# Kernel optimization log

Hardware: AMD Instinct MI355X
Metric: run time of the kernel (lower is better)

The kernel has to match this reference:

```python
import jax, jax.numpy as jnp
import numpy as np

N = 20000      # nodes
E = 160000     # edges (before self-loops)
B = 128        # graphs in batch
NEG_SLOPE = 0.2


def gat_layer(x, src, dst, W, a_src, a_dst, b):
    # x: [N, Cin]; W: [Cin, H*C]; a_src/a_dst: [H, C]; b: [C]
    H, C = a_src.shape
    n = x.shape[0]
    xw = (x @ W).reshape(n, H, C)                      # [N, H, C]
    alpha_src = jnp.sum(xw * a_src, axis=-1)           # [N, H]
    alpha_dst = jnp.sum(xw * a_dst, axis=-1)           # [N, H]
    e = jax.nn.leaky_relu(alpha_src[src] + alpha_dst[dst], NEG_SLOPE)  # [Etot, H]
    # numerically stable segment softmax over edges grouped by target node
    m = jax.ops.segment_max(e, dst, num_segments=n)    # [N, H]
    m = jnp.where(jnp.isfinite(m), m, 0.0)
    ex = jnp.exp(e - m[dst])                           # [Etot, H]
    den = jax.ops.segment_sum(ex, dst, num_segments=n) # [N, H]
    alpha = ex / (den[dst] + 1e-16)                    # [Etot, H]
    out = jax.ops.segment_sum(alpha[:, :, None] * xw[src], dst, num_segments=n)  # [N, H, C]
    return out.mean(axis=1) + b                        # concat=False -> head mean + bias


def setup_inputs() -> dict:
    key = jax.random.key(0)
    ks = jax.random.split(key, 12)
    s = 0.05
    x = jax.random.normal(ks[0], (N, 768), dtype=jnp.float32)
    edge_index = jax.random.randint(ks[1], (2, E), 0, N, dtype=jnp.int64)
    batch = jnp.sort(jax.random.randint(ks[2], (N,), 0, B, dtype=jnp.int64))
    W1 = jax.random.normal(ks[3], (768, 4 * 512), dtype=jnp.float32) * s
    a_src1 = jax.random.normal(ks[4], (4, 512), dtype=jnp.float32) * s
    a_dst1 = jax.random.normal(ks[5], (4, 512), dtype=jnp.float32) * s
    b1 = jnp.zeros((512,), dtype=jnp.float32)
    W2 = jax.random.normal(ks[6], (512, 4 * 256), dtype=jnp.float32) * s
    a_src2 = jax.random.normal(ks[7], (4, 256), dtype=jnp.float32) * s
    a_dst2 = jax.random.normal(ks[8], (4, 256), dtype=jnp.float32) * s
    b2 = jnp.zeros((256,), dtype=jnp.float32)
    fcW = jax.random.normal(ks[9], (256, 2), dtype=jnp.float32) * s
    fcb = jnp.zeros((2,), dtype=jnp.float32)
    return {"x": x, "edge_index": edge_index, "batch": batch,
            "W1": W1, "a_src1": a_src1, "a_dst1": a_dst1, "b1": b1,
            "W2": W2, "a_src2": a_src2, "a_dst2": a_dst2, "b2": b2,
            "fcW": fcW, "fcb": fcb}


def reference(x, edge_index, batch, W1, a_src1, a_dst1, b1, W2, a_src2, a_dst2, b2, fcW, fcb):
    n = x.shape[0]
    loops = jnp.arange(n, dtype=edge_index.dtype)      # GATConv adds self-loops by default
    src = jnp.concatenate([edge_index[0], loops])
    dst = jnp.concatenate([edge_index[1], loops])
    h = gat_layer(x, src, dst, W1, a_src1, a_dst1, b1)   # [N, 512]
    h = gat_layer(h, src, dst, W2, a_src2, a_dst2, b2)   # [N, 256]
    sums = jax.ops.segment_sum(h, batch, num_segments=B)                     # [B, 256]
    cnt = jax.ops.segment_sum(jnp.ones((n,), h.dtype), batch, num_segments=B)
    g = sums / jnp.maximum(cnt, 1.0)[:, None]            # scatter_mean
    return g @ fcW + fcb                                  # [B, 2]
```

## Files before the change

### kernel.cpp

```cpp
#include <hip/hip_runtime.h>

#define NN    20000
#define NE    160000
#define NETOT 180000
#define NB    128

typedef __attribute__((ext_vector_type(4))) float f32x4;
typedef __attribute__((ext_vector_type(8))) short s16x8;

__device__ __forceinline__ unsigned short f2bf(float f){
  unsigned u = __float_as_uint(f);
  return (unsigned short)((u + 0x7FFFu + ((u >> 16) & 1u)) >> 16);
}
__device__ __forceinline__ float bf2f(unsigned short h){
  return __uint_as_float(((unsigned)h) << 16);
}
__device__ __forceinline__ void gload16(const void* g, void* l){
  __builtin_amdgcn_global_load_lds((const __attribute__((address_space(1))) void*)g,
                                   (__attribute__((address_space(3))) void*)l, 16, 0, 0);
}

__global__ void k_cvt(const float* __restrict__ in, unsigned short* __restrict__ outp, int n4){
  int i = blockIdx.x * blockDim.x + threadIdx.x;
  if (i >= n4) return;
  float4 v = ((const float4*)in)[i];
  ushort4 h;
  h.x = f2bf(v.x); h.y = f2bf(v.y); h.z = f2bf(v.z); h.w = f2bf(v.w);
  ((ushort4*)outp)[i] = h;
}

__global__ void k_tcvt(const float* __restrict__ W, unsigned short* __restrict__ T, int K, int N){
  __shared__ float tile[32][33];
  int tx = threadIdx.x, ty = threadIdx.y;
  int n = blockIdx.x * 32 + tx, k = blockIdx.y * 32 + ty;
  tile[ty][tx] = W[(size_t)k * N + n];
  __syncthreads();
  int n2 = blockIdx.x * 32 + ty, k2 = blockIdx.y * 32 + tx;
  T[(size_t)n2 * K + k2] = f2bf(tile[tx][ty]);
}

__global__ __launch_bounds__(256, 2)
void gemm_bf16(const unsigned short* __restrict__ A, const unsigned short* __restrict__ BT,
               unsigned short* __restrict__ C, int M, int N, int K, int ntile){
  __shared__ unsigned short lds[24576];
  const int t = threadIdx.x;
  const int lane = t & 63;
  const int w = t >> 6;
  const int wr = w >> 1, wc = w & 1;
  const int mt = blockIdx.x / ntile, nt = blockIdx.x % ntile;
  const int m0 = mt << 7, n0 = nt << 8;
  const int NK = K >> 5;

  int offA[4], offB[8];
#pragma unroll
  for (int mi = 0; mi < 4; ++mi){
    int row = wr * 64 + mi * 16 + (lane & 15);
    offA[mi] = row * 32 + (((lane >> 4) ^ ((row >> 1) & 3)) << 3);
  }
#pragma unroll
  for (int ni = 0; ni < 8; ++ni){
    int row = wc * 128 + ni * 16 + (lane & 15);
    offB[ni] = 4096 + row * 32 + (((lane >> 4) ^ ((row >> 1) & 3)) << 3);
  }

  const unsigned short* srcA[2]; int dstA[2];
#pragma unroll
  for (int j = 0; j < 2; ++j){
    int rA = w * 32 + j * 16 + (lane >> 2);
    int gr = m0 + rA; if (gr >= M) gr = M - 1;
    srcA[j] = A + (size_t)gr * K + (((lane & 3) ^ ((rA >> 1) & 3)) << 3);
    dstA[j] = w * 1024 + j * 512 + lane * 8;
  }
  const unsigned short* srcB[4]; int dstB[4];
#pragma unroll
  for (int j = 0; j < 4; ++j){
    int rB = w * 64 + j * 16 + (lane >> 2);
    srcB[j] = BT + (size_t)(n0 + rB) * K + (((lane & 3) ^ ((rB >> 1) & 3)) << 3);
    dstB[j] = 4096 + w * 2048 + j * 512 + lane * 8;
  }

#define STAGE(ks, bo) { int _k = (ks) << 5; \
    gload16(srcA[0] + _k, &lds[(bo) + dstA[0]]); \
    gload16(srcA[1] + _k, &lds[(bo) + dstA[1]]); \
    gload16(srcB[0] + _k, &lds[(bo) + dstB[0]]); \
    gload16(srcB[1] + _k, &lds[(bo) + dstB[1]]); \
    gload16(srcB[2] + _k, &lds[(bo) + dstB[2]]); \
    gload16(srcB[3] + _k, &lds[(bo) + dstB[3]]); }

  f32x4 acc[4][8];
#pragma unroll
  for (int i = 0; i < 4; ++i)
#pragma unroll
    for (int j = 0; j < 8; ++j) acc[i][j] = (f32x4){0.f, 0.f, 0.f, 0.f};

  STAGE(0, 0);
  asm volatile("s_waitcnt vmcnt(0)" ::: "memory");
  __builtin_amdgcn_sched_barrier(0);
  __builtin_amdgcn_s_barrier();
  __builtin_amdgcn_sched_barrier(0);

  for (int ks = 0; ks < NK; ++ks){
    const int bo = (ks & 1) * 12288;
    s16x8 av[4], bv[8];
#pragma unroll
    for (int i = 0; i < 4; ++i) av[i] = *(const s16x8*)&lds[bo + offA[i]];
#pragma unroll
    for (int i = 0; i < 8; ++i) bv[i] = *(const s16x8*)&lds[bo + offB[i]];
    if (ks + 1 < NK) STAGE(ks + 1, 12288 - bo);
    __builtin_amdgcn_s_setprio(1);
#pragma unroll
    for (int mi = 0; mi < 4; ++mi)
#pragma unroll
      for (int ni = 0; ni < 8; ++ni)
        acc[mi][ni] = __builtin_amdgcn_mfma_f32_16x16x32_bf16(av[mi], bv[ni], acc[mi][ni], 0, 0, 0);
    __builtin_amdgcn_s_setprio(0);
    asm volatile("s_waitcnt vmcnt(0)" ::: "memory");
    __builtin_amdgcn_sched_barrier(0);
    __builtin_amdgcn_s_barrier();
    __builtin_amdgcn_sched_barrier(0);
  }
#undef STAGE

#pragma unroll
  for (int h = 0; h < 2; ++h){
    if (wr == h){
#pragma unroll
      for (int mi = 0; mi < 4; ++mi)
#pragma unroll
        for (int ni = 0; ni < 8; ++ni)
#pragma unroll
          for (int r = 0; r < 4; ++r){
            int rl = mi * 16 + ((lane >> 4) << 2) + r;
            int col = wc * 128 + ni * 16 + (lane & 15);
            int byte = (rl * 512 + col * 2) ^ (((rl >> 2) & 3) << 5);
            *(unsigned short*)((char*)lds + byte) = f2bf(acc[mi][ni][r]);
          }
    }
    __syncthreads();
#pragma unroll
    for (int it = 0; it < 8; ++it){
      int idx = it * 256 + t;
      int rl = idx >> 5, c16 = idx & 31;
      int byte = (rl * 512 + c16 * 16) ^ (((rl >> 2) & 3) << 5);
      s16x8 v = *(const s16x8*)((const char*)lds + byte);
      int grow = m0 + h * 64 + rl;
      if (grow < M)
        *(s16x8*)(C + (size_t)grow * N + n0 + c16 * 8) = v;
    }
    __syncthreads();
  }
}

template<int C>
__global__ void k_alpha(const unsigned short* __restrict__ xw, const float* __restrict__ a_src,
                        const float* __restrict__ a_dst, float* __restrict__ asrc,
                        float* __restrict__ adst){
  const int n = blockIdx.x, t = threadIdx.x;
  constexpr int W = C / 8;
  const int head = (t * 8) / C;
  const int c0 = (t * 8) % C;
  s16x8 v = *(const s16x8*)(xw + (size_t)n * 4 * C + t * 8);
  float4 s0 = *(const float4*)(a_src + head * C + c0);
  float4 s1 = *(const float4*)(a_src + head * C + c0 + 4);
  float4 d0 = *(const float4*)(a_dst + head * C + c0);
  float4 d1 = *(const float4*)(a_dst + head * C + c0 + 4);
  float f[8];
#pragma unroll
  for (int j = 0; j < 8; ++j) f[j] = bf2f((unsigned short)v[j]);
  float ps = f[0]*s0.x + f[1]*s0.y + f[2]*s0.z + f[3]*s0.w
           + f[4]*s1.x + f[5]*s1.y + f[6]*s1.z + f[7]*s1.w;
  float pd = f[0]*d0.x + f[1]*d0.y + f[2]*d0.z + f[3]*d0.w
           + f[4]*d1.x + f[5]*d1.y + f[6]*d1.z + f[7]*d1.w;
#pragma unroll
  for (int off = W / 2; off; off >>= 1){
    ps += __shfl_xor(ps, off);
    pd += __shfl_xor(pd, off);
  }
  if ((t & (W - 1)) == 0){
    asrc[n * 4 + head] = ps;
    adst[n * 4 + head] = pd;
  }
}

__global__ void k_count(const int* __restrict__ ei, int* __restrict__ counts){
  int e = blockIdx.x * blockDim.x + threadIdx.x;
  if (e >= NETOT) return;
  int d = (e < NE) ? ei[NE + e] : (e - NE);
  atomicAdd(&counts[d], 1);
}
__global__ void k_scan(const int* __restrict__ counts, int* __restrict__ row_ptr,
                       int* __restrict__ cursor){
  __shared__ int lds[1024];
  int t = threadIdx.x;
  int base = 0;
  for (int c0 = 0; c0 < NN; c0 += 1024){
    int i = c0 + t;
    int v = (i < NN) ? counts[i] : 0;
    __syncthreads();
    lds[t] = v;
    __syncthreads();
    for (int off = 1; off < 1024; off <<= 1){
      int x = (t >= off) ? lds[t - off] : 0;
      __syncthreads();
      lds[t] += x;
      __syncthreads();
    }
    int excl = base + lds[t] - v;
    if (i < NN){ row_ptr[i] = excl; cursor[i] = excl; }
    base += lds[1023];
  }
  if (t == 0) row_ptr[NN] = base;
}
__global__ void k_scatter(const int* __restrict__ ei, int* __restrict__ cursor,
                          int* __restrict__ csr_src){
  int e = blockIdx.x * blockDim.x + threadIdx.x;
  if (e >= NETOT) return;
  int s, d;
  if (e < NE){ s = ei[e]; d = ei[NE + e]; } else { s = d = e - NE; }
  int pos = atomicAdd(&cursor[d], 1);
  csr_src[pos] = s;
}

__global__ void k_edge(const int* __restrict__ rp, const int* __restrict__ csrc,
                       const float* __restrict__ asrc, const float* __restrict__ adst,
                       float* __restrict__ ex, float* __restrict__ den){
  int n = blockIdx.x * 4 + (threadIdx.x >> 6);
  if (n >= NN) return;
  int lane = threadIdx.x & 63;
  int beg = rp[n], end = rp[n + 1];
  float4 ad = ((const float4*)adst)[n];
  float mx0 = -1e30f, mx1 = -1e30f, mx2 = -1e30f, mx3 = -1e30f;
  for (int i = beg + lane; i < end; i += 64){
    int s = csrc[i];
    float4 as = ((const float4*)asrc)[s];
    float v0 = as.x + ad.x; v0 = v0 > 0.f ? v0 : 0.2f * v0; mx0 = fmaxf(mx0, v0);
    float v1 = as.y + ad.y; v1 = v1 > 0.f ? v1 : 0.2f * v1; mx1 = fmaxf(mx1, v1);
    float v2 = as.z + ad.z; v2 = v2 > 0.f ? v2 : 0.2f * v2; mx2 = fmaxf(mx2, v2);
    float v3 = as.w + ad.w; v3 = v3 > 0.f ? v3 : 0.2f * v3; mx3 = fmaxf(mx3, v3);
  }
#pragma unroll
  for (int off = 32; off; off >>= 1){
    mx0 = fmaxf(mx0, __shfl_xor(mx0, off));
    mx1 = fmaxf(mx1, __shfl_xor(mx1, off));
    mx2 = fmaxf(mx2, __shfl_xor(mx2, off));
    mx3 = fmaxf(mx3, __shfl_xor(mx3, off));
  }
  float s0 = 0.f, s1 = 0.f, s2 = 0.f, s3 = 0.f;
  for (int i = beg + lane; i < end; i += 64){
    int s = csrc[i];
    float4 as = ((const float4*)asrc)[s];
    float v0 = as.x + ad.x; v0 = v0 > 0.f ? v0 : 0.2f * v0;
    float v1 = as.y + ad.y; v1 = v1 > 0.f ? v1 : 0.2f * v1;
    float v2 = as.z + ad.z; v2 = v2 > 0.f ? v2 : 0.2f * v2;
    float v3 = as.w + ad.w; v3 = v3 > 0.f ? v3 : 0.2f * v3;
    float e0 = __expf(v0 - mx0), e1 = __expf(v1 - mx1);
    float e2 = __expf(v2 - mx2), e3 = __expf(v3 - mx3);
    s0 += e0; s1 += e1; s2 += e2; s3 += e3;
    ((float4*)ex)[i] = make_float4(e0, e1, e2, e3);
  }
#pragma unroll
  for (int off = 32; off; off >>= 1){
    s0 += __shfl_xor(s0, off);
    s1 += __shfl_xor(s1, off);
    s2 += __shfl_xor(s2, off);
    s3 += __shfl_xor(s3, off);
  }
  if (lane == 0) ((float4*)den)[n] = make_float4(s0, s1, s2, s3);
}

template<int C, bool BF16OUT>
__global__ void k_agg(const unsigned short* __restrict__ xw, const int* __restrict__ row_ptr,
                      const int* __restrict__ csr_src,
                      const float* __restrict__ ex, const float* __restrict__ den,
                      const float* __restrict__ bias, void* __restrict__ outp){
  const int n = blockIdx.x, t = threadIdx.x;
  constexpr int LPH = C / 8;
  const int h = t / LPH, c0 = (t % LPH) * 8;
  __shared__ float red[4][C];
  float rdh = 1.f / (den[n * 4 + h] + 1e-16f);
  float acc[8] = {};
  int beg = row_ptr[n], end = row_ptr[n + 1];
  const unsigned short* xwh = xw + h * C + c0;
  for (int i = beg; i < end; ++i){
    int s = csr_src[i];
    float aa = ex[i * 4 + h] * rdh;
    s16x8 v = *(const s16x8*)(xwh + (size_t)s * 4 * C);
#pragma unroll
    for (int j = 0; j < 8; ++j) acc[j] += aa * bf2f((unsigned short)v[j]);
  }
#pragma unroll
  for (int j = 0; j < 8; ++j) red[h][c0 + j] = acc[j];
  __syncthreads();
  if (t < LPH){
    int cc = t * 8;
    float o[8];
#pragma unroll
    for (int j = 0; j < 8; ++j)
      o[j] = 0.25f * (red[0][cc + j] + red[1][cc + j] + red[2][cc + j] + red[3][cc + j])
           + bias[cc + j];
    if (BF16OUT){
      union { unsigned short u[8]; s16x8 v; } pk;
#pragma unroll
      for (int j = 0; j < 8; ++j) pk.u[j] = f2bf(o[j]);
      *(s16x8*)((unsigned short*)outp + (size_t)n * C + cc) = pk.v;
    } else {
      float* op = (float*)outp + (size_t)n * C + cc;
      ((float4*)op)[0] = make_float4(o[0], o[1], o[2], o[3]);
      ((float4*)op)[1] = make_float4(o[4], o[5], o[6], o[7]);
    }
  }
}

__global__ void k_pool(const float* __restrict__ h2, const int* __restrict__ batch,
                       float* __restrict__ sums, int* __restrict__ cnt){
  int n0 = blockIdx.x * 64;
  int t = threadIdx.x;
  int nend = n0 + 64; if (nend > NN) nend = NN;
  int cur = batch[n0];
  float acc = 0.f; int run = 0;
  for (int n = n0; n < nend; ++n){
    int b = batch[n];
    if (b != cur){
      atomicAdd(&sums[cur * 256 + t], acc);
      if (t == 0) atomicAdd(&cnt[cur], run);
      acc = 0.f; run = 0; cur = b;
    }
    acc += h2[(size_t)n * 256 + t];
    run++;
  }
  atomicAdd(&sums[cur * 256 + t], acc);
  if (t == 0) atomicAdd(&cnt[cur], run);
}

__global__ void k_fc(const float* __restrict__ sums, const int* __restrict__ cnt,
                     const float* __restrict__ fcW, const float* __restrict__ fcb,
                     float* __restrict__ out){
  int b = blockIdx.x, t = threadIdx.x;
  int c = cnt[b]; if (c < 1) c = 1;
  float inv = 1.f / (float)c;
  float v = sums[b * 256 + t] * inv;
  float p0 = v * fcW[t * 2];
  float p1 = v * fcW[t * 2 + 1];
#pragma unroll
  for (int off = 32; off; off >>= 1){
    p0 += __shfl_xor(p0, off);
    p1 += __shfl_xor(p1, off);
  }
  __shared__ float r0[4], r1[4];
  if ((t & 63) == 0){ r0[t >> 6] = p0; r1[t >> 6] = p1; }
  __syncthreads();
  if (t == 0){
    out[b * 2 + 0] = r0[0] + r0[1] + r0[2] + r0[3] + fcb[0];
    out[b * 2 + 1] = r1[0] + r1[1] + r1[2] + r1[3] + fcb[1];
  }
}

extern "C" void kernel_launch(void* const* d_in, const int* in_sizes, int n_in,
                              void* d_out, int out_size, void* d_ws, size_t ws_size,
                              hipStream_t stream){
  const float* x      = (const float*)d_in[0];
  const int*   ei     = (const int*)d_in[1];
  const int*   batch  = (const int*)d_in[2];
  const float* W1     = (const float*)d_in[3];
  const float* a_src1 = (const float*)d_in[4];
  const float* a_dst1 = (const float*)d_in[5];
  const float* b1     = (const float*)d_in[6];
  const float* W2     = (const float*)d_in[7];
  const float* a_src2 = (const float*)d_in[8];
  const float* a_dst2 = (const float*)d_in[9];
  const float* b2     = (const float*)d_in[10];
  const float* fcW    = (const float*)d_in[11];
  const float* fcb    = (const float*)d_in[12];
  float* out = (float*)d_out;
  (void)in_sizes; (void)n_in; (void)out_size; (void)ws_size;

  char* ws = (char*)d_ws;
  size_t off = 0;
  auto take = [&](size_t bytes) -> char* {
    char* p = ws + off;
    off += (bytes + 255) & ~(size_t)255;
    return p;
  };
  char* slab0 = take(81920000);
  unsigned short* xw1 = (unsigned short*)slab0;
  unsigned short* xw2 = (unsigned short*)slab0;
  unsigned short* x_bf  = (unsigned short*)take(30720000);
  unsigned short* h1_bf = (unsigned short*)take(20480000);
  float*          h2    = (float*)take(20480000);
  unsigned short* W1T = (unsigned short*)take(3145728);
  unsigned short* W2T = (unsigned short*)take(1048576);
  float* asrc   = (float*)take(320000);
  float* adst   = (float*)take(320000);
  float* den    = (float*)take(320000);
  float* ex     = (float*)take((size_t)NETOT * 16);
  int* counts   = (int*)take(80004);
  int* row_ptr  = (int*)take(80004);
  int* cursor   = (int*)take(80004);
  int* csr_src  = (int*)take(720000);
  float* sums   = (float*)take(131072);
  int* cnt      = (int*)take(512);

  const int egrid = (NETOT + 255) / 256;

  hipMemsetAsync(counts, 0, NN * 4, stream);
  k_count<<<egrid, 256, 0, stream>>>(ei, counts);
  k_scan<<<1, 1024, 0, stream>>>(counts, row_ptr, cursor);
  k_scatter<<<egrid, 256, 0, stream>>>(ei, cursor, csr_src);

  k_cvt<<<(3840000 + 255) / 256, 256, 0, stream>>>(x, x_bf, 3840000);
  k_tcvt<<<dim3(2048 / 32, 768 / 32), dim3(32, 32), 0, stream>>>(W1, W1T, 768, 2048);
  gemm_bf16<<<157 * 8, 256, 0, stream>>>(x_bf, W1T, xw1, NN, 2048, 768, 8);
  k_alpha<512><<<NN, 256, 0, stream>>>(xw1, a_src1, a_dst1, asrc, adst);
  k_edge<<<(NN + 3) / 4, 256, 0, stream>>>(row_ptr, csr_src, asrc, adst, ex, den);
  k_agg<512, true><<<NN, 256, 0, stream>>>(xw1, row_ptr, csr_src, ex, den, b1, h1_bf);

  k_tcvt<<<dim3(1024 / 32, 512 / 32), dim3(32, 32), 0, stream>>>(W2, W2T, 512, 1024);
  gemm_bf16<<<157 * 4, 256, 0, stream>>>(h1_bf, W2T, xw2, NN, 1024, 512, 4);
  k_alpha<256><<<NN, 128, 0, stream>>>(xw2, a_src2, a_dst2, asrc, adst);
  k_edge<<<(NN + 3) / 4, 256, 0, stream>>>(row_ptr, csr_src, asrc, adst, ex, den);
  k_agg<256, false><<<NN, 128, 0, stream>>>(xw2, row_ptr, csr_src, ex, den, b2, h2);

  hipMemsetAsync(sums, 0, 131072, stream);
  hipMemsetAsync(cnt, 0, 512, stream);
  k_pool<<<(NN + 63) / 64, 256, 0, stream>>>(h2, batch, sums, cnt);
  k_fc<<<NB, 256, 0, stream>>>(sums, cnt, fcW, fcb, out);
}
```

Before: 540.2 us.

## Aggregate raw inputs per head before projecting, folding head-mean into GEMM

Reorders each GAT layer algebraically. Attention logits come from x·(W·a), so a small projected vector replaces the full x@W. Aggregation runs on the raw input features per head (width 4·Cin). A single GEMM with a head-concatenated weight scaled by 0.25 and a fused bias then performs the head mean. This drops the ex/den buffers and the separate edge and alpha passes, and fuses the softmax into aggregation. In exchange the aggregated intermediate is larger (N×4·Cin in bf16), the GEMM K grows, and the GEMM grid for layer 2 has only 157 blocks. The layer-2 output is also stored in bf16, which costs precision.

```diff
diff --git a/kernel.cpp b/kernel.cpp
--- a/kernel.cpp
+++ b/kernel.cpp
@@ -29,156 +29,66 @@
   ((ushort4*)outp)[i] = h;
 }
 
-__global__ void k_tcvt(const float* __restrict__ W, unsigned short* __restrict__ T, int K, int N){
-  __shared__ float tile[32][33];
-  int tx = threadIdx.x, ty = threadIdx.y;
-  int n = blockIdx.x * 32 + tx, k = blockIdx.y * 32 + ty;
-  tile[ty][tx] = W[(size_t)k * N + n];
+__global__ void k_va(const float* __restrict__ W, const float* __restrict__ aS,
+                     const float* __restrict__ aD, float* __restrict__ va, int K, int C){
+  __shared__ float a_s[2048], a_d[2048];
+  int t = threadIdx.x;
+  int HC = 4 * C;
+  for (int i = t; i < HC; i += 256){ a_s[i] = aS[i]; a_d[i] = aD[i]; }
   __syncthreads();
-  int n2 = blockIdx.x * 32 + ty, k2 = blockIdx.y * 32 + tx;
-  T[(size_t)n2 * K + k2] = f2bf(tile[tx][ty]);
-}
-
-__global__ __launch_bounds__(256, 2)
-void gemm_bf16(const unsigned short* __restrict__ A, const unsigned short* __restrict__ BT,
-               unsigned short* __restrict__ C, int M, int N, int K, int ntile){
-  __shared__ unsigned short lds[24576];
-  const int t = threadIdx.x;
-  const int lane = t & 63;
-  const int w = t >> 6;
-  const int wr = w >> 1, wc = w & 1;
-  const int mt = blockIdx.x / ntile, nt = blockIdx.x % ntile;
-  const int m0 = mt << 7, n0 = nt << 8;
-  const int NK = K >> 5;
-
-  int offA[4], offB[8];
-#pragma unroll
-  for (int mi = 0; mi < 4; ++mi){
-    int row = wr * 64 + mi * 16 + (lane & 15);
-    offA[mi] = row * 32 + (((lane >> 4) ^ ((row >> 1) & 3)) << 3);
-  }
-#pragma unroll
-  for (int ni = 0; ni < 8; ++ni){
-    int row = wc * 128 + ni * 16 + (lane & 15);
-    offB[ni] = 4096 + row * 32 + (((lane >> 4) ^ ((row >> 1) & 3)) << 3);
-  }
-
-  const unsigned short* srcA[2]; int dstA[2];
-#pragma unroll
-  for (int j = 0; j < 2; ++j){
-    int rA = w * 32 + j * 16 + (lane >> 2);
-    int gr = m0 + rA; if (gr >= M) gr = M - 1;
-    srcA[j] = A + (size_t)gr * K + (((lane & 3) ^ ((rA >> 1) & 3)) << 3);
-    dstA[j] = w * 1024 + j * 512 + lane * 8;
-  }
-  const unsigned short* srcB[4]; int dstB[4];
-#pragma unroll
-  for (int j = 0; j < 4; ++j){
-    int rB = w * 64 + j * 16 + (lane >> 2);
-    srcB[j] = BT + (size_t)(n0 + rB) * K + (((lane & 3) ^ ((rB >> 1) & 3)) << 3);
-    dstB[j] = 4096 + w * 2048 + j * 512 + lane * 8;
-  }
-
-#define STAGE(ks, bo) { int _k = (ks) << 5; \
-    gload16(srcA[0] + _k, &lds[(bo) + dstA[0]]); \
-    gload16(srcA[1] + _k, &lds[(bo) + dstA[1]]); \
-    gload16(srcB[0] + _k, &lds[(bo) + dstB[0]]); \
-    gload16(srcB[1] + _k, &lds[(bo) + dstB[1]]); \
-    gload16(srcB[2] + _k, &lds[(bo) + dstB[2]]); \
-    gload16(srcB[3] + _k, &lds[(bo) + dstB[3]]); }
-
-  f32x4 acc[4][8];
-#pragma unroll
-  for (int i = 0; i < 4; ++i)
-#pragma unroll
-    for (int j = 0; j < 8; ++j) acc[i][j] = (f32x4){0.f, 0.f, 0.f, 0.f};
-
-  STAGE(0, 0);
-  asm volatile("s_waitcnt vmcnt(0)" ::: "memory");
-  __builtin_amdgcn_sched_barrier(0);
-  __builtin_amdgcn_s_barrier();
-  __builtin_amdgcn_sched_barrier(0);
-
-  for (int ks = 0; ks < NK; ++ks){
-    const int bo = (ks & 1) * 12288;
-    s16x8 av[4], bv[8];
-#pragma unroll
-    for (int i = 0; i < 4; ++i) av[i] = *(const s16x8*)&lds[bo + offA[i]];
-#pragma unroll
-    for (int i = 0; i < 8; ++i) bv[i] = *(const s16x8*)&lds[bo + offB[i]];
-    if (ks + 1 < NK) STAGE(ks + 1, 12288 - bo);
-    __builtin_amdgcn_s_setprio(1);
-#pragma unroll
-    for (int mi = 0; mi < 4; ++mi)
-#pragma unroll
-      for (int ni = 0; ni < 8; ++ni)
-        acc[mi][ni] = __builtin_amdgcn_mfma_f32_16x16x32_bf16(av[mi], bv[ni], acc[mi][ni], 0, 0, 0);
-    __builtin_amdgcn_s_setprio(0);
-    asm volatile("s_waitcnt vmcnt(0)" ::: "memory");
-    __builtin_amdgcn_sched_barrier(0);
-    __builtin_amdgcn_s_barrier();
-    __builtin_amdgcn_sched_barrier(0);
-  }
-#undef STAGE
-
-#pragma unroll
-  for (int h = 0; h < 2; ++h){
-    if (wr == h){
-#pragma unroll
-      for (int mi = 0; mi < 4; ++mi)
-#pragma unroll
-        for (int ni = 0; ni < 8; ++ni)
-#pragma unroll
-          for (int r = 0; r < 4; ++r){
-            int rl = mi * 16 + ((lane >> 4) << 2) + r;
-            int col = wc * 128 + ni * 16 + (lane & 15);
-            int byte = (rl * 512 + col * 2) ^ (((rl >> 2) & 3) << 5);
-            *(unsigned short*)((char*)lds + byte) = f2bf(acc[mi][ni][r]);
-          }
-    }
-    __syncthreads();
-#pragma unroll
-    for (int it = 0; it < 8; ++it){
-      int idx = it * 256 + t;
-      int rl = idx >> 5, c16 = idx & 31;
-      int byte = (rl * 512 + c16 * 16) ^ (((rl >> 2) & 3) << 5);
-      s16x8 v = *(const s16x8*)((const char*)lds + byte);
-      int grow = m0 + h * 64 + rl;
-      if (grow < M)
-        *(s16x8*)(C + (size_t)grow * N + n0 + c16 * 8) = v;
-    }
-    __syncthreads();
-  }
-}
-
-template<int C>
-__global__ void k_alpha(const unsigned short* __restrict__ xw, const float* __restrict__ a_src,
-                        const float* __restrict__ a_dst, float* __restrict__ asrc,
-                        float* __restrict__ adst){
-  const int n = blockIdx.x, t = threadIdx.x;
-  constexpr int W = C / 8;
-  const int head = (t * 8) / C;
-  const int c0 = (t * 8) % C;
-  s16x8 v = *(const s16x8*)(xw + (size_t)n * 4 * C + t * 8);
-  float4 s0 = *(const float4*)(a_src + head * C + c0);
-  float4 s1 = *(const float4*)(a_src + head * C + c0 + 4);
-  float4 d0 = *(const float4*)(a_dst + head * C + c0);
-  float4 d1 = *(const float4*)(a_dst + head * C + c0 + 4);
-  float f[8];
-#pragma unroll
-  for (int j = 0; j < 8; ++j) f[j] = bf2f((unsigned short)v[j]);
-  float ps = f[0]*s0.x + f[1]*s0.y + f[2]*s0.z + f[3]*s0.w
-           + f[4]*s1.x + f[5]*s1.y + f[6]*s1.z + f[7]*s1.w;
-  float pd = f[0]*d0.x + f[1]*d0.y + f[2]*d0.z + f[3]*d0.w
-           + f[4]*d1.x + f[5]*d1.y + f[6]*d1.z + f[7]*d1.w;
-#pragma unroll
-  for (int off = W / 2; off; off >>= 1){
-    ps += __shfl_xor(ps, off);
-    pd += __shfl_xor(pd, off);
-  }
-  if ((t & (W - 1)) == 0){
-    asrc[n * 4 + head] = ps;
-    adst[n * 4 + head] = pd;
+  int k = blockIdx.x * 4 + (t >> 6);
+  int lane = t & 63;
+  if (k >= K) return;
+  float ss[4] = {0.f,0.f,0.f,0.f}, dd[4] = {0.f,0.f,0.f,0.f};
+  for (int h = 0; h < 4; ++h)
+    for (int c0 = 0; c0 < C; c0 += 64){
+      float wv = W[(size_t)k * HC + h * C + c0 + lane];
+      ss[h] += wv * a_s[h * C + c0 + lane];
+      dd[h] += wv * a_d[h * C + c0 + lane];
+    }
+#pragma unroll
+  for (int off = 32; off; off >>= 1)
+#pragma unroll
+    for (int h = 0; h < 4; ++h){
+      ss[h] += __shfl_xor(ss[h], off);
+      dd[h] += __shfl_xor(dd[h], off);
+    }
+  if (lane == 0)
+#pragma unroll
+    for (int h = 0; h < 4; ++h){
+      va[h * K + k] = ss[h];
+      va[(4 + h) * K + k] = dd[h];
+    }
+}
+
+template<int K>
+__global__ void k_alpha_in(const unsigned short* __restrict__ xf, const float* __restrict__ va,
+                           float* __restrict__ asrc, float* __restrict__ adst){
+  __shared__ float v_s[8 * K];
+  int t = threadIdx.x;
+  for (int i = t; i < 8 * K; i += 256) v_s[i] = va[i];
+  __syncthreads();
+  int n = blockIdx.x * 4 + (t >> 6);
+  if (n >= NN) return;
+  int lane = t & 63;
+  const unsigned short* xr = xf + (size_t)n * K;
+  float s[8] = {};
+#pragma unroll
+  for (int j = 0; j < K / 128; ++j){
+    int idx = j * 128 + lane * 2;
+    ushort2 xv = *(const ushort2*)(xr + idx);
+    float f0 = bf2f(xv.x), f1 = bf2f(xv.y);
+#pragma unroll
+    for (int a = 0; a < 8; ++a)
+      s[a] += f0 * v_s[a * K + idx] + f1 * v_s[a * K + idx + 1];
+  }
+#pragma unroll
+  for (int off = 32; off; off >>= 1)
+#pragma unroll
+    for (int a = 0; a < 8; ++a) s[a] += __shfl_xor(s[a], off);
+  if (lane == 0){
+    ((float4*)asrc)[n] = make_float4(s[0], s[1], s[2], s[3]);
+    ((float4*)adst)[n] = make_float4(s[4], s[5], s[6], s[7]);
   }
 }
 
@@ -221,97 +131,211 @@
   csr_src[pos] = s;
 }
 
-__global__ void k_edge(const int* __restrict__ rp, const int* __restrict__ csrc,
-                       const float* __restrict__ asrc, const float* __restrict__ adst,
-                       float* __restrict__ ex, float* __restrict__ den){
-  int n = blockIdx.x * 4 + (threadIdx.x >> 6);
-  if (n >= NN) return;
-  int lane = threadIdx.x & 63;
+template<int K>
+__global__ void k_aggx(const unsigned short* __restrict__ xf, const int* __restrict__ rp,
+                       const int* __restrict__ csrc, const float* __restrict__ asrc,
+                       const float* __restrict__ adst, unsigned short* __restrict__ agg){
+  const int n = blockIdx.x, t = threadIdx.x;
+  __shared__ float sm[4], srd[4];
   int beg = rp[n], end = rp[n + 1];
   float4 ad = ((const float4*)adst)[n];
-  float mx0 = -1e30f, mx1 = -1e30f, mx2 = -1e30f, mx3 = -1e30f;
-  for (int i = beg + lane; i < end; i += 64){
+  if (t < 64){
+    float m0 = -1e30f, m1 = -1e30f, m2 = -1e30f, m3 = -1e30f;
+    for (int i = beg + t; i < end; i += 64){
+      int s = csrc[i];
+      float4 as = ((const float4*)asrc)[s];
+      float v0 = as.x + ad.x; v0 = v0 > 0.f ? v0 : 0.2f * v0; m0 = fmaxf(m0, v0);
+      float v1 = as.y + ad.y; v1 = v1 > 0.f ? v1 : 0.2f * v1; m1 = fmaxf(m1, v1);
+      float v2 = as.z + ad.z; v2 = v2 > 0.f ? v2 : 0.2f * v2; m2 = fmaxf(m2, v2);
+      float v3 = as.w + ad.w; v3 = v3 > 0.f ? v3 : 0.2f * v3; m3 = fmaxf(m3, v3);
+    }
+#pragma unroll
+    for (int off = 32; off; off >>= 1){
+      m0 = fmaxf(m0, __shfl_xor(m0, off));
+      m1 = fmaxf(m1, __shfl_xor(m1, off));
+      m2 = fmaxf(m2, __shfl_xor(m2, off));
+      m3 = fmaxf(m3, __shfl_xor(m3, off));
+    }
+    float s0 = 0.f, s1 = 0.f, s2 = 0.f, s3 = 0.f;
+    for (int i = beg + t; i < end; i += 64){
+      int s = csrc[i];
+      float4 as = ((const float4*)asrc)[s];
+      float v0 = as.x + ad.x; v0 = v0 > 0.f ? v0 : 0.2f * v0;
+      float v1 = as.y + ad.y; v1 = v1 > 0.f ? v1 : 0.2f * v1;
+      float v2 = as.z + ad.z; v2 = v2 > 0.f ? v2 : 0.2f * v2;
+      float v3 = as.w + ad.w; v3 = v3 > 0.f ? v3 : 0.2f * v3;
+      s0 += __expf(v0 - m0); s1 += __expf(v1 - m1);
+      s2 += __expf(v2 - m2); s3 += __expf(v3 - m3);
+    }
+#pragma unroll
+    for (int off = 32; off; off >>= 1){
+      s0 += __shfl_xor(s0, off); s1 += __shfl_xor(s1, off);
+      s2 += __shfl_xor(s2, off); s3 += __shfl_xor(s3, off);
+    }
+    if (t == 0){
+      sm[0] = m0; sm[1] = m1; sm[2] = m2; sm[3] = m3;
+      srd[0] = 1.f / (s0 + 1e-16f); srd[1] = 1.f / (s1 + 1e-16f);
+      srd[2] = 1.f / (s2 + 1e-16f); srd[3] = 1.f / (s3 + 1e-16f);
+    }
+  }
+  __syncthreads();
+  float m0 = sm[0], m1 = sm[1], m2 = sm[2], m3 = sm[3];
+  float r0 = srd[0], r1 = srd[1], r2 = srd[2], r3 = srd[3];
+  float acc[4][4] = {};
+  for (int i = beg; i < end; ++i){
     int s = csrc[i];
     float4 as = ((const float4*)asrc)[s];
-    float v0 = as.x + ad.x; v0 = v0 > 0.f ? v0 : 0.2f * v0; mx0 = fmaxf(mx0, v0);
-    float v1 = as.y + ad.y; v1 = v1 > 0.f ? v1 : 0.2f * v1; mx1 = fmaxf(mx1, v1);
-    float v2 = as.z + ad.z; v2 = v2 > 0.f ? v2 : 0.2f * v2; mx2 = fmaxf(mx2, v2);
-    float v3 = as.w + ad.w; v3 = v3 > 0.f ? v3 : 0.2f * v3; mx3 = fmaxf(mx3, v3);
-  }
-#pragma unroll
-  for (int off = 32; off; off >>= 1){
-    mx0 = fmaxf(mx0, __shfl_xor(mx0, off));
-    mx1 = fmaxf(mx1, __shfl_xor(mx1, off));
-    mx2 = fmaxf(mx2, __shfl_xor(mx2, off));
-    mx3 = fmaxf(mx3, __shfl_xor(mx3, off));
-  }
-  float s0 = 0.f, s1 = 0.f, s2 = 0.f, s3 = 0.f;
-  for (int i = beg + lane; i < end; i += 64){
-    int s = csrc[i];
-    float4 as = ((const float4*)asrc)[s];
-    float v0 = as.x + ad.x; v0 = v0 > 0.f ? v0 : 0.2f * v0;
-    float v1 = as.y + ad.y; v1 = v1 > 0.f ? v1 : 0.2f * v1;
-    float v2 = as.z + ad.z; v2 = v2 > 0.f ? v2 : 0.2f * v2;
-    float v3 = as.w + ad.w; v3 = v3 > 0.f ? v3 : 0.2f * v3;
-    float e0 = __expf(v0 - mx0), e1 = __expf(v1 - mx1);
-    float e2 = __expf(v2 - mx2), e3 = __expf(v3 - mx3);
-    s0 += e0; s1 += e1; s2 += e2; s3 += e3;
-    ((float4*)ex)[i] = make_float4(e0, e1, e2, e3);
-  }
-#pragma unroll
-  for (int off = 32; off; off >>= 1){
-    s0 += __shfl_xor(s0, off);
-    s1 += __shfl_xor(s1, off);
-    s2 += __shfl_xor(s2, off);
-    s3 += __shfl_xor(s3, off);
-  }
-  if (lane == 0) ((float4*)den)[n] = make_float4(s0, s1, s2, s3);
-}
-
-template<int C, bool BF16OUT>
-__global__ void k_agg(const unsigned short* __restrict__ xw, const int* __restrict__ row_ptr,
-                      const int* __restrict__ csr_src,
-                      const float* __restrict__ ex, const float* __restrict__ den,
-                      const float* __restrict__ bias, void* __restrict__ outp){
-  const int n = blockIdx.x, t = threadIdx.x;
-  constexpr int LPH = C / 8;
-  const int h = t / LPH, c0 = (t % LPH) * 8;
-  __shared__ float red[4][C];
-  float rdh = 1.f / (den[n * 4 + h] + 1e-16f);
-  float acc[8] = {};
-  int beg = row_ptr[n], end = row_ptr[n + 1];
-  const unsigned short* xwh = xw + h * C + c0;
-  for (int i = beg; i < end; ++i){
-    int s = csr_src[i];
-    float aa = ex[i * 4 + h] * rdh;
-    s16x8 v = *(const s16x8*)(xwh + (size_t)s * 4 * C);
-#pragma unroll
-    for (int j = 0; j < 8; ++j) acc[j] += aa * bf2f((unsigned short)v[j]);
-  }
-#pragma unroll
-  for (int j = 0; j < 8; ++j) red[h][c0 + j] = acc[j];
+    float v0 = as.x + ad.x; v0 = v0 > 0.f ? v0 : 0.2f * v0; float a0 = __expf(v0 - m0) * r0;
+    float v1 = as.y + ad.y; v1 = v1 > 0.f ? v1 : 0.2f * v1; float a1 = __expf(v1 - m1) * r1;
+    float v2 = as.z + ad.z; v2 = v2 > 0.f ? v2 : 0.2f * v2; float a2 = __expf(v2 - m2) * r2;
+    float v3 = as.w + ad.w; v3 = v3 > 0.f ? v3 : 0.2f * v3; float a3 = __expf(v3 - m3) * r3;
+    ushort4 xv = *(const ushort4*)(xf + (size_t)s * K + 4 * t);
+    float f0 = bf2f(xv.x), f1 = bf2f(xv.y), f2 = bf2f(xv.z), f3 = bf2f(xv.w);
+    acc[0][0] += a0 * f0; acc[0][1] += a0 * f1; acc[0][2] += a0 * f2; acc[0][3] += a0 * f3;
+    acc[1][0] += a1 * f0; acc[1][1] += a1 * f1; acc[1][2] += a1 * f2; acc[1][3] += a1 * f3;
+    acc[2][0] += a2 * f0; acc[2][1] += a2 * f1; acc[2][2] += a2 * f2; acc[2][3] += a2 * f3;
+    acc[3][0] += a3 * f0; acc[3][1] += a3 * f1; acc[3][2] += a3 * f2; acc[3][3] += a3 * f3;
+  }
+#pragma unroll
+  for (int h = 0; h < 4; ++h){
+    ushort4 pk;
+    pk.x = f2bf(acc[h][0]); pk.y = f2bf(acc[h][1]);
+    pk.z = f2bf(acc[h][2]); pk.w = f2bf(acc[h][3]);
+    *(ushort4*)(agg + (size_t)n * 4 * K + h * K + 4 * t) = pk;
+  }
+}
+
+__global__ void k_tcvt_cat(const float* __restrict__ W, unsigned short* __restrict__ T,
+                           int K, int C){
+  __shared__ float tile[32][33];
+  int tx = threadIdx.x, ty = threadIdx.y;
+  int h = blockIdx.z;
+  int c = blockIdx.x * 32 + tx, k = blockIdx.y * 32 + ty;
+  tile[ty][tx] = W[(size_t)k * (4 * C) + h * C + c];
   __syncthreads();
-  if (t < LPH){
-    int cc = t * 8;
-    float o[8];
-#pragma unroll
-    for (int j = 0; j < 8; ++j)
-      o[j] = 0.25f * (red[0][cc + j] + red[1][cc + j] + red[2][cc + j] + red[3][cc + j])
-           + bias[cc + j];
-    if (BF16OUT){
-      union { unsigned short u[8]; s16x8 v; } pk;
-#pragma unroll
-      for (int j = 0; j < 8; ++j) pk.u[j] = f2bf(o[j]);
-      *(s16x8*)((unsigned short*)outp + (size_t)n * C + cc) = pk.v;
-    } else {
-      float* op = (float*)outp + (size_t)n * C + cc;
-      ((float4*)op)[0] = make_float4(o[0], o[1], o[2], o[3]);
-      ((float4*)op)[1] = make_float4(o[4], o[5], o[6], o[7]);
-    }
-  }
-}
-
-__global__ void k_pool(const float* __restrict__ h2, const int* __restrict__ batch,
+  int c2 = blockIdx.x * 32 + ty, k2 = blockIdx.y * 32 + tx;
+  T[(size_t)c2 * (4 * K) + h * K + k2] = f2bf(0.25f * tile[tx][ty]);
+}
+
+__global__ __launch_bounds__(256, 2)
+void gemm_bf16(const unsigned short* __restrict__ A, const unsigned short* __restrict__ BT,
+               const float* __restrict__ bias, unsigned short* __restrict__ C,
+               int M, int N, int K, int ntile){
+  __shared__ unsigned short lds[24576];
+  const int t = threadIdx.x;
+  const int lane = t & 63;
+  const int w = t >> 6;
+  const int wr = w >> 1, wc = w & 1;
+  const int mt = blockIdx.x / ntile, nt = blockIdx.x % ntile;
+  const int m0 = mt << 7, n0 = nt << 8;
+  const int NK = K >> 5;
+
+  int offA[4], offB[8];
+#pragma unroll
+  for (int mi = 0; mi < 4; ++mi){
+    int row = wr * 64 + mi * 16 + (lane & 15);
+    offA[mi] = row * 32 + (((lane >> 4) ^ ((row >> 1) & 3)) << 3);
+  }
+#pragma unroll
+  for (int ni = 0; ni < 8; ++ni){
+    int row = wc * 128 + ni * 16 + (lane & 15);
+    offB[ni] = 4096 + row * 32 + (((lane >> 4) ^ ((row >> 1) & 3)) << 3);
+  }
+
+  const unsigned short* srcA[2]; int dstA[2];
+#pragma unroll
+  for (int j = 0; j < 2; ++j){
+    int rA = w * 32 + j * 16 + (lane >> 2);
+    int gr = m0 + rA; if (gr >= M) gr = M - 1;
+    srcA[j] = A + (size_t)gr * K + (((lane & 3) ^ ((rA >> 1) & 3)) << 3);
+    dstA[j] = w * 1024 + j * 512 + lane * 8;
+  }
+  const unsigned short* srcB[4]; int dstB[4];
+#pragma unroll
+  for (int j = 0; j < 4; ++j){
+    int rB = w * 64 + j * 16 + (lane >> 2);
+    srcB[j] = BT + (size_t)(n0 + rB) * K + (((lane & 3) ^ ((rB >> 1) & 3)) << 3);
+    dstB[j] = 4096 + w * 2048 + j * 512 + lane * 8;
+  }
+
+#define STAGE(ks, bo) { int _k = (ks) << 5; \
+    gload16(srcA[0] + _k, &lds[(bo) + dstA[0]]); \
+    gload16(srcA[1] + _k, &lds[(bo) + dstA[1]]); \
+    gload16(srcB[0] + _k, &lds[(bo) + dstB[0]]); \
+    gload16(srcB[1] + _k, &lds[(bo) + dstB[1]]); \
+    gload16(srcB[2] + _k, &lds[(bo) + dstB[2]]); \
+    gload16(srcB[3] + _k, &lds[(bo) + dstB[3]]); }
+
+  f32x4 acc[4][8];
+#pragma unroll
+  for (int i = 0; i < 4; ++i)
+#pragma unroll
+    for (int j = 0; j < 8; ++j) acc[i][j] = (f32x4){0.f, 0.f, 0.f, 0.f};
+
+  STAGE(0, 0);
+  asm volatile("s_waitcnt vmcnt(0)" ::: "memory");
+  __builtin_amdgcn_sched_barrier(0);
+  __builtin_amdgcn_s_barrier();
+  __builtin_amdgcn_sched_barrier(0);
+
+  for (int ks = 0; ks < NK; ++ks){
+    const int bo = (ks & 1) * 12288;
+    s16x8 av[4], bv[8];
+#pragma unroll
+    for (int i = 0; i < 4; ++i) av[i] = *(const s16x8*)&lds[bo + offA[i]];
+#pragma unroll
+    for (int i = 0; i < 8; ++i) bv[i] = *(const s16x8*)&lds[bo + offB[i]];
+    if (ks + 1 < NK) STAGE(ks + 1, 12288 - bo);
+    __builtin_amdgcn_s_setprio(1);
+#pragma unroll
+    for (int mi = 0; mi < 4; ++mi)
+#pragma unroll
+      for (int ni = 0; ni < 8; ++ni)
+        acc[mi][ni] = __builtin_amdgcn_mfma_f32_16x16x32_bf16(av[mi], bv[ni], acc[mi][ni], 0, 0, 0);
+    __builtin_amdgcn_s_setprio(0);
+    asm volatile("s_waitcnt vmcnt(0)" ::: "memory");
+    __builtin_amdgcn_sched_barrier(0);
+    __builtin_amdgcn_s_barrier();
+    __builtin_amdgcn_sched_barrier(0);
+  }
+#undef STAGE
+
+  float bb[8];
+#pragma unroll
+  for (int ni = 0; ni < 8; ++ni)
+    bb[ni] = bias[n0 + wc * 128 + ni * 16 + (lane & 15)];
+
+#pragma unroll
+  for (int h = 0; h < 2; ++h){
+    if (wr == h){
+#pragma unroll
+      for (int mi = 0; mi < 4; ++mi)
+#pragma unroll
+        for (int ni = 0; ni < 8; ++ni)
+#pragma unroll
+          for (int r = 0; r < 4; ++r){
+            int rl = mi * 16 + ((lane >> 4) << 2) + r;
+            int col = wc * 128 + ni * 16 + (lane & 15);
+            int byte = (rl * 512 + col * 2) ^ (((rl >> 2) & 3) << 5);
+            *(unsigned short*)((char*)lds + byte) = f2bf(acc[mi][ni][r] + bb[ni]);
+          }
+    }
+    __syncthreads();
+#pragma unroll
+    for (int it = 0; it < 8; ++it){
+      int idx = it * 256 + t;
+      int rl = idx >> 5, c16 = idx & 31;
+      int byte = (rl * 512 + c16 * 16) ^ (((rl >> 2) & 3) << 5);
+      s16x8 v = *(const s16x8*)((const char*)lds + byte);
+      int grow = m0 + h * 64 + rl;
+      if (grow < M)
+        *(s16x8*)(C + (size_t)grow * N + n0 + c16 * 8) = v;
+    }
+    __syncthreads();
+  }
+}
+
+__global__ void k_pool(const unsigned short* __restrict__ h2, const int* __restrict__ batch,
                        float* __restrict__ sums, int* __restrict__ cnt){
   int n0 = blockIdx.x * 64;
   int t = threadIdx.x;
@@ -325,7 +349,7 @@
       if (t == 0) atomicAdd(&cnt[cur], run);
       acc = 0.f; run = 0; cur = b;
     }
-    acc += h2[(size_t)n * 256 + t];
+    acc += bf2f(h2[(size_t)n * 256 + t]);
     run++;
   }
   atomicAdd(&sums[cur * 256 + t], acc);
@@ -381,18 +405,18 @@
     off += (bytes + 255) & ~(size_t)255;
     return p;
   };
-  char* slab0 = take(81920000);
-  unsigned short* xw1 = (unsigned short*)slab0;
-  unsigned short* xw2 = (unsigned short*)slab0;
-  unsigned short* x_bf  = (unsigned short*)take(30720000);
+  char* slabA = take(122880000);
+  unsigned short* agg1 = (unsigned short*)slabA;
+  unsigned short* agg2 = (unsigned short*)slabA;
+  char* slabB = take(30720000);
+  unsigned short* x_bf  = (unsigned short*)slabB;
+  unsigned short* h2_bf = (unsigned short*)slabB;
   unsigned short* h1_bf = (unsigned short*)take(20480000);
-  float*          h2    = (float*)take(20480000);
-  unsigned short* W1T = (unsigned short*)take(3145728);
-  unsigned short* W2T = (unsigned short*)take(1048576);
+  unsigned short* Wc1T  = (unsigned short*)take(3145728);
+  unsigned short* Wc2T  = (unsigned short*)take(1048576);
+  float* va     = (float*)take(24576);
   float* asrc   = (float*)take(320000);
   float* adst   = (float*)take(320000);
-  float* den    = (float*)take(320000);
-  float* ex     = (float*)take((size_t)NETOT * 16);
   int* counts   = (int*)take(80004);
   int* row_ptr  = (int*)take(80004);
   int* cursor   = (int*)take(80004);
@@ -408,20 +432,20 @@
   k_scatter<<<egrid, 256, 0, stream>>>(ei, cursor, csr_src);
 
   k_cvt<<<(3840000 + 255) / 256, 256, 0, stream>>>(x, x_bf, 3840000);
-  k_tcvt<<<dim3(2048 / 32, 768 / 32), dim3(32, 32), 0, stream>>>(W1, W1T, 768, 2048);
-  gemm_bf16<<<157 * 8, 256, 0, stream>>>(x_bf, W1T, xw1, NN, 2048, 768, 8);
-  k_alpha<512><<<NN, 256, 0, stream>>>(xw1, a_src1, a_dst1, asrc, adst);
-  k_edge<<<(NN + 3) / 4, 256, 0, stream>>>(row_ptr, csr_src, asrc, adst, ex, den);
-  k_agg<512, true><<<NN, 256, 0, stream>>>(xw1, row_ptr, csr_src, ex, den, b1, h1_bf);
-
-  k_tcvt<<<dim3(1024 / 32, 512 / 32), dim3(32, 32), 0, stream>>>(W2, W2T, 512, 1024);
-  gemm_bf16<<<157 * 4, 256, 0, stream>>>(h1_bf, W2T, xw2, NN, 1024, 512, 4);
-  k_alpha<256><<<NN, 128, 0, stream>>>(xw2, a_src2, a_dst2, asrc, adst);
-  k_edge<<<(NN + 3) / 4, 256, 0, stream>>>(row_ptr, csr_src, asrc, adst, ex, den);
-  k_agg<256, false><<<NN, 128, 0, stream>>>(xw2, row_ptr, csr_src, ex, den, b2, h2);
+  k_va<<<192, 256, 0, stream>>>(W1, a_src1, a_dst1, va, 768, 512);
+  k_alpha_in<768><<<NN / 4, 256, 0, stream>>>(x_bf, va, asrc, adst);
+  k_tcvt_cat<<<dim3(16, 24, 4), dim3(32, 32), 0, stream>>>(W1, Wc1T, 768, 512);
+  k_aggx<768><<<NN, 192, 0, stream>>>(x_bf, row_ptr, csr_src, asrc, adst, agg1);
+  gemm_bf16<<<157 * 2, 256, 0, stream>>>(agg1, Wc1T, b1, h1_bf, NN, 512, 3072, 2);
+
+  k_va<<<128, 256, 0, stream>>>(W2, a_src2, a_dst2, va, 512, 256);
+  k_alpha_in<512><<<NN / 4, 256, 0, stream>>>(h1_bf, va, asrc, adst);
+  k_tcvt_cat<<<dim3(8, 16, 4), dim3(32, 32), 0, stream>>>(W2, Wc2T, 512, 256);
+  k_aggx<512><<<NN, 128, 0, stream>>>(h1_bf, row_ptr, csr_src, asrc, adst, agg2);
+  gemm_bf16<<<157 * 1, 256, 0, stream>>>(agg2, Wc2T, b2, h2_bf, NN, 256, 2048, 1);
 
   hipMemsetAsync(sums, 0, 131072, stream);
   hipMemsetAsync(cnt, 0, 512, stream);
-  k_pool<<<(NN + 63) / 64, 256, 0, stream>>>(h2, batch, sums, cnt);
+  k_pool<<<(NN + 63) / 64, 256, 0, stream>>>(h2_bf, batch, sums, cnt);
   k_fc<<<NB, 256, 0, stream>>>(sums, cnt, fcW, fcb, out);
 }
```

Measured after the change: 518.0 us. -4.1%, faster.
